# Kernel optimization log

Hardware: AMD Instinct MI355X
Metric: run time of the kernel (lower is better)

The kernel has to match this reference:

```python
import jax, jax.numpy as jnp
import numpy as np

B, N, D_IN = 16, 2048, 256
C, H = 32, 64          # num_capsules, dim_capsules
HEADS, KD = 4, 64      # attention heads, key_dim = dim_capsules
ROUTINGS = 3
EPS_SQ = 1e-7
LN_EPS = 1e-3


def squash(v, axis=-1):
    s2 = jnp.sum(jnp.square(v), axis=axis, keepdims=True)
    scale = s2 / (1.0 + s2) / jnp.sqrt(s2 + EPS_SQ)
    return scale * v


def setup_inputs() -> dict:
    key = jax.random.key(0)
    ks = jax.random.split(key, 10)
    # VarianceScaling(scale=2.0, fan_avg, uniform) for W
    fan_avg = (D_IN + H) / 2.0
    limit = float(np.sqrt(3.0 * 2.0 / fan_avg))
    W = jax.random.uniform(ks[0], (C, D_IN, H), minval=-limit, maxval=limit, dtype=jnp.float32)
    b_caps = jnp.zeros((C, H), jnp.float32)
    gamma = jnp.full((1,), 3.0, jnp.float32)
    x = jax.random.normal(ks[1], (B, N, D_IN), dtype=jnp.float32)
    def glorot(k, shape):
        fin, fout = shape[0], int(np.prod(shape[1:]))
        lim = float(np.sqrt(6.0 / (fin + fout)))
        return jax.random.uniform(k, shape, minval=-lim, maxval=lim, dtype=jnp.float32)
    Wq = glorot(ks[2], (H, HEADS, KD)); bq = jnp.zeros((HEADS, KD), jnp.float32)
    Wk = glorot(ks[3], (H, HEADS, KD)); bk = jnp.zeros((HEADS, KD), jnp.float32)
    Wv = glorot(ks[4], (H, HEADS, KD)); bv = jnp.zeros((HEADS, KD), jnp.float32)
    Wo = glorot(ks[5], (HEADS, KD, H)); bo = jnp.zeros((H,), jnp.float32)
    ln_gamma = jnp.ones((H,), jnp.float32)
    ln_beta = jnp.zeros((H,), jnp.float32)
    return dict(x=x, W=W, b_caps=b_caps, gamma=gamma,
                Wq=Wq, bq=bq, Wk=Wk, bk=bk, Wv=Wv, bv=bv, Wo=Wo, bo=bo,
                ln_gamma=ln_gamma, ln_beta=ln_beta)


def dynamic_routing(u_hat):
    # u_hat: [B, N, C, H]
    b = jnp.zeros(u_hat.shape[:3] + (1,), u_hat.dtype)
    v = None
    for i in range(ROUTINGS):
        c = jax.nn.softmax(b, axis=2)                      # [B,N,C,1]
        s = jnp.sum(c * u_hat, axis=1, keepdims=True)      # [B,1,C,H]
        v = squash(s, axis=-1)
        if i < ROUTINGS - 1:
            agreement = jnp.sum(u_hat * v, axis=-1, keepdims=True)
            b = b + agreement
    return jnp.squeeze(v, axis=1)                          # [B,C,H]


def mha_self(xq, Wq, bq, Wk, bk, Wv, bv, Wo, bo):
    # xq: [B, C, H]
    q = jnp.einsum('bch,hnk->bcnk', xq, Wq) + bq
    k = jnp.einsum('bch,hnk->bcnk', xq, Wk) + bk
    v = jnp.einsum('bch,hnk->bcnk', xq, Wv) + bv
    scores = jnp.einsum('bqnd,bknd->bnqk', q, k) / jnp.sqrt(jnp.asarray(KD, xq.dtype))
    attn = jax.nn.softmax(scores, axis=-1)
    ctx = jnp.einsum('bnqk,bknd->bqnd', attn, v)
    return jnp.einsum('bqnd,ndh->bqh', ctx, Wo) + bo


def reference(x, W, b_caps, gamma, Wq, bq, Wk, bk, Wv, bv, Wo, bo, ln_gamma, ln_beta):
    u_hat = jnp.einsum('bnd,cdh->bnch', x, W) + b_caps[None, None]  # [B,N,C,H]
    routed = dynamic_routing(u_hat)                                  # [B,C,H]
    attended = mha_self(routed, Wq, bq, Wk, bk, Wv, bv, Wo, bo)
    y = attended + routed
    mu = jnp.mean(y, axis=-1, keepdims=True)
    var = jnp.mean(jnp.square(y - mu), axis=-1, keepdims=True)
    routed = (y - mu) / jnp.sqrt(var + LN_EPS) * ln_gamma + ln_beta
    return squash(routed, axis=-1) * gamma
```

## Files before the change

### kernel.cpp

```cpp
#include <hip/hip_runtime.h>
#include <cstddef>

typedef _Float16 f16;
typedef __attribute__((ext_vector_type(4))) _Float16 f16x4;
typedef __attribute__((ext_vector_type(8))) _Float16 f16x8;
typedef __attribute__((ext_vector_type(4))) float f32x4;

namespace {
constexpr int kB = 16;
constexpr int kN = 2048;
constexpr int kD = 256;
constexpr int kC = 32;
constexpr int kH = 64;
constexpr int kHeads = 4;
constexpr int kKD = 64;
constexpr int kChunks = 32;
constexpr int kRows = kN / kChunks;
constexpr int kXJ = 64;

constexpr size_t OFF_XPART = 0;
constexpr size_t OFF_V     = OFF_XPART + 262144;
constexpr size_t OFF_WV    = OFF_V + 32768;
constexpr size_t OFF_BV    = OFF_WV + 131072;
constexpr size_t OFF_Y     = OFF_BV + 512;
constexpr size_t OFF_CS    = OFF_Y + 131072;
constexpr size_t OFF_QKV   = OFF_CS + 512;
constexpr size_t OFF_CTX   = OFF_QKV + 393216;
constexpr size_t OFF_XF16  = OFF_CTX + 524288;
constexpr size_t OFF_WVH   = OFF_XF16 + 4194304;
constexpr size_t OFF_CSP   = OFF_WVH + 65536;
constexpr size_t OFF_YP    = OFF_CSP + 16384;
constexpr size_t WS_NEED_PARTIAL = (OFF_YP + 4194304) * sizeof(float);
}

__global__ __launch_bounds__(256) void k_xpart(const float* __restrict__ x,
                                               float* __restrict__ xpart,
                                               f16* __restrict__ xh) {
  const int b = blockIdx.x, j = blockIdx.y;
  const int t = threadIdx.x;
  const int rg = t >> 6, dq = t & 63;
  __shared__ float sL[4][kD];
  float4 s = {0.f, 0.f, 0.f, 0.f};
  const size_t rowbase = (size_t)b * kN + (size_t)j * 32;
#pragma unroll
  for (int i = 0; i < 8; ++i) {
    const int r = rg * 8 + i;
    const float4 q = *(reinterpret_cast<const float4*>(x + (rowbase + r) * kD) + dq);
    s.x += q.x; s.y += q.y; s.z += q.z; s.w += q.w;
    f16x4 h4 = {(f16)q.x, (f16)q.y, (f16)q.z, (f16)q.w};
    *(reinterpret_cast<f16x4*>(xh + (rowbase + r) * kD) + dq) = h4;
  }
  reinterpret_cast<float4*>(&sL[rg][0])[dq] = s;
  __syncthreads();
  const int d = t;
  xpart[((size_t)b * kXJ + j) * kD + d] =
      sL[0][d] + sL[1][d] + sL[2][d] + sL[3][d];
}

__global__ __launch_bounds__(256) void k_sv(
    const float* __restrict__ W, const float* __restrict__ b_caps,
    const float* __restrict__ xpart, const float* __restrict__ y,
    const float* __restrict__ csum, const float* __restrict__ ypart,
    const float* __restrict__ cspart, float* __restrict__ v,
    float* __restrict__ Wv, f16* __restrict__ Wvh, float* __restrict__ bv,
    const int mode, const int computeWv, const int accWv, const int npart) {
  const int bc = blockIdx.x, b = bc >> 5, c = bc & 31;
  const int t = threadIdx.x;
  const int w = t >> 6, h = t & 63;
  __shared__ float yL[kD];
  __shared__ float sL[4][kH];
  __shared__ float vL[kH];
  __shared__ float csLs;

  if (mode == 0) {
    float s = 0.f;
#pragma unroll 8
    for (int j = 0; j < kXJ; ++j) s += xpart[((size_t)b * kXJ + j) * kD + t];
    yL[t] = s * (1.f / (float)kC);
    if (t == 0) csLs = (float)kN / (float)kC;
  } else if (npart > 0) {
    float s = 0.f;
#pragma unroll 8
    for (int ch = 0; ch < kChunks; ++ch)
      s += ypart[(((size_t)b * kChunks + ch) * kC + c) * kD + t];
    yL[t] = s;
    if (t < 32) {
      float cs_ = cspart[((size_t)b * kChunks + t) * kC + c];
#pragma unroll
      for (int off = 16; off; off >>= 1) cs_ += __shfl_xor(cs_, off, 64);
      if (t == 0) csLs = cs_;
    }
  } else {
    yL[t] = y[(size_t)bc * kD + t];
    if (t == 0) csLs = csum[bc];
  }
  __syncthreads();

  const float* Wc = W + (size_t)c * kD * kH;
  {
    float acc = 0.f;
#pragma unroll 8
    for (int d = w * 64; d < (w + 1) * 64; ++d)
      acc = fmaf(yL[d], Wc[(size_t)d * kH + h], acc);
    sL[w][h] = acc;
  }
  __syncthreads();

  if (t < 64) {
    const float bch = b_caps[c * kH + h];
    float s = sL[0][h] + sL[1][h] + sL[2][h] + sL[3][h] + csLs * bch;
    float s2 = s * s;
#pragma unroll
    for (int off = 32; off; off >>= 1) s2 += __shfl_xor(s2, off, 64);
    const float scale = s2 / (1.f + s2) * rsqrtf(s2 + 1e-7f);
    const float vh = scale * s;
    v[(size_t)bc * kH + h] = vh;
    vL[h] = vh;
    if (computeWv) {
      float bvp = bch * vh;
#pragma unroll
      for (int off = 32; off; off >>= 1) bvp += __shfl_xor(bvp, off, 64);
      if (h == 0) bv[bc] = accWv ? (bv[bc] + bvp) : bvp;
    }
  }
  __syncthreads();
  if (computeWv) {
    float acc = 0.f;
    const float* Wrow = Wc + (size_t)t * kH;
#pragma unroll 8
    for (int hh = 0; hh < kH; ++hh) acc = fmaf(Wrow[hh], vL[hh], acc);
    const size_t idx = (size_t)bc * kD + t;
    const float nv = accWv ? (Wv[idx] + acc) : acc;
    Wv[idx] = nv;
    Wvh[idx] = (f16)nv;
  }
}

__global__ __launch_bounds__(256) void k_route(
    const f16* __restrict__ xh, const f16* __restrict__ Wvh,
    const float* __restrict__ bv, float* __restrict__ y,
    float* __restrict__ csum, float* __restrict__ ypart,
    float* __restrict__ cspart, const int usePart) {
  const int b = blockIdx.x, chunk = blockIdx.y;
  const int t = threadIdx.x;
  const int lane = t & 63, w = t >> 6;
  const int l15 = lane & 15, q = lane >> 4;

  __shared__ __align__(16) f16 xsT[kD][kRows + 8];
  __shared__ float aL[kRows][kC + 4];
  __shared__ __align__(16) f16 pT[kC][kRows + 8];
  __shared__ float csL[8][kC];

  const int n0 = chunk * kRows;
  const float bvc = bv[b * kC + (t & 31)];

  f32x4 acc0 = {0.f, 0.f, 0.f, 0.f}, acc1 = {0.f, 0.f, 0.f, 0.f};
  {
    const int row = w * 16 + l15;
    const f16x8* Ar = reinterpret_cast<const f16x8*>(
        xh + ((size_t)(b * kN + n0 + row)) * kD + q * 8);
    const f16x8* B0 = reinterpret_cast<const f16x8*>(
        Wvh + ((size_t)(b * kC + l15)) * kD + q * 8);
    const f16x8* B1 = reinterpret_cast<const f16x8*>(
        Wvh + ((size_t)(b * kC + 16 + l15)) * kD + q * 8);
#pragma unroll
    for (int ks = 0; ks < 8; ++ks) {
      f16x8 af = Ar[ks * 4];
      acc0 = __builtin_amdgcn_mfma_f32_16x16x32_f16(af, B0[ks * 4], acc0, 0, 0, 0);
      acc1 = __builtin_amdgcn_mfma_f32_16x16x32_f16(af, B1[ks * 4], acc1, 0, 0, 0);
      const int dbase = ks * 32 + q * 8;
#pragma unroll
      for (int i = 0; i < 8; ++i) {
        const int ii = (i + 2 * q) & 7;
        xsT[dbase + ii][row] = af[ii];
      }
    }
  }
#pragma unroll
  for (int r = 0; r < 4; ++r) {
    aL[w * 16 + q * 4 + r][l15] = acc0[r];
    aL[w * 16 + q * 4 + r][16 + l15] = acc1[r];
  }
  __syncthreads();

  const int c = t & 31, sg = t >> 5;
  float csreg = 0.f;
#pragma unroll
  for (int k = 0; k < 8; ++k) {
    const int r = sg * 8 + k;
    float L = bvc + aL[r][c];
    float m = L;
#pragma unroll
    for (int off = 16; off; off >>= 1) m = fmaxf(m, __shfl_xor(m, off, 64));
    const float e = __expf(L - m);
    float ssum = e;
#pragma unroll
    for (int off = 16; off; off >>= 1) ssum += __shfl_xor(ssum, off, 64);
    const float p = e / ssum;
    pT[c][r] = (f16)p;
    csreg += p;
  }
  csL[sg][c] = csreg;
  __syncthreads();

  const int mt2 = w & 1;
  const int ntb = (w >> 1) * 8;
  const f16x8 a0 = *reinterpret_cast<const f16x8*>(&pT[mt2 * 16 + l15][q * 8]);
  const f16x8 a1 = *reinterpret_cast<const f16x8*>(&pT[mt2 * 16 + l15][32 + q * 8]);
  const int cap = mt2 * 16 + q * 4;
#pragma unroll
  for (int i = 0; i < 8; ++i) {
    const int d0 = (ntb + i) * 16;
    const f16x8 b0 = *reinterpret_cast<const f16x8*>(&xsT[d0 + l15][q * 8]);
    const f16x8 b1 = *reinterpret_cast<const f16x8*>(&xsT[d0 + l15][32 + q * 8]);
    f32x4 o = {0.f, 0.f, 0.f, 0.f};
    o = __builtin_amdgcn_mfma_f32_16x16x32_f16(a0, b0, o, 0, 0, 0);
    o = __builtin_amdgcn_mfma_f32_16x16x32_f16(a1, b1, o, 0, 0, 0);
    if (usePart) {
      float* dst = ypart + (((size_t)(b * kChunks + chunk)) * kC + cap) * kD + d0 + l15;
#pragma unroll
      for (int r = 0; r < 4; ++r) dst[(size_t)r * kD] = o[r];
    } else {
      float* dst = y + ((size_t)(b * kC + cap)) * kD + d0 + l15;
#pragma unroll
      for (int r = 0; r < 4; ++r) atomicAdd(dst + (size_t)r * kD, o[r]);
    }
  }
  if (t < 32) {
    float s = 0.f;
#pragma unroll
    for (int j = 0; j < 8; ++j) s += csL[j][t];
    if (usePart) cspart[((size_t)b * kChunks + chunk) * kC + t] = s;
    else atomicAdd(csum + b * kC + t, s);
  }
}

__global__ __launch_bounds__(256) void k_qkv(
    const float* __restrict__ routed, const float* __restrict__ Wq,
    const float* __restrict__ bq, const float* __restrict__ Wk,
    const float* __restrict__ bk, const float* __restrict__ Wvp,
    const float* __restrict__ bvp, float* __restrict__ qkv) {
  const int b = blockIdx.x, head = blockIdx.y, which = blockIdx.z;
  const int t = threadIdx.x;
  const int kk = t & 63, w = t >> 6;
  const float* Wsrc = (which == 0) ? Wq : (which == 1) ? Wk : Wvp;
  const float* bsrc = (which == 0) ? bq : (which == 1) ? bk : bvp;
  __shared__ float rL[kC * kH];
#pragma unroll
  for (int i = 0; i < 8; ++i) rL[t + 256 * i] = routed[(size_t)b * kC * kH + t + 256 * i];
  __syncthreads();
  float acc[8];
  const float bb = bsrc[head * kKD + kk];
#pragma unroll
  for (int i = 0; i < 8; ++i) acc[i] = bb;
#pragma unroll 4
  for (int hh = 0; hh < kH; ++hh) {
    const float wv = Wsrc[((size_t)hh * kHeads + head) * kKD + kk];
#pragma unroll
    for (int i = 0; i < 8; ++i)
      acc[i] = fmaf(rL[(w + 4 * i) * kH + hh], wv, acc[i]);
  }
#pragma unroll
  for (int i = 0; i < 8; ++i) {
    const int cc = w + 4 * i;
    qkv[((((size_t)which * kB + b) * kHeads + head) * kC + cc) * kKD + kk] = acc[i];
  }
}

__global__ __launch_bounds__(256) void k_attn2(const float* __restrict__ qkv,
                                               float* __restrict__ ctx) {
  const int b = blockIdx.x, head = blockIdx.y, t = threadIdx.x;
  constexpr size_t kWhichStride = (size_t)kB * kHeads * kC * kKD;
  const size_t base = ((size_t)b * kHeads + head) * kC * kKD;
  __shared__ float qL[kC][kKD];
  __shared__ float kL[kC][kKD + 1];
  __shared__ float vL[kC][kKD];
  __shared__ float sc[kC][kC + 1];
#pragma unroll
  for (int i = 0; i < 8; ++i) {
    const int e = t + 256 * i, cc = e >> 6, kk = e & 63;
    qL[cc][kk] = qkv[base + e];
    kL[cc][kk] = qkv[base + kWhichStride + e];
    vL[cc][kk] = qkv[base + 2 * kWhichStride + e];
  }
  __syncthreads();
#pragma unroll
  for (int i = 0; i < 4; ++i) {
    const int e = t + 256 * i, qc = e >> 5, kc = e & 31;
    float s = 0.f;
#pragma unroll 8
    for (int d = 0; d < kKD; ++d) s = fmaf(qL[qc][d], kL[kc][d], s);
    sc[qc][kc] = s * 0.125f;
  }
  __syncthreads();
  if (t < kC) {
    float m = -1e30f;
#pragma unroll
    for (int kc = 0; kc < kC; ++kc) m = fmaxf(m, sc[t][kc]);
    float ssum = 0.f;
#pragma unroll
    for (int kc = 0; kc < kC; ++kc) {
      const float e2 = __expf(sc[t][kc] - m);
      sc[t][kc] = e2;
      ssum += e2;
    }
    const float inv = 1.f / ssum;
#pragma unroll
    for (int kc = 0; kc < kC; ++kc) sc[t][kc] *= inv;
  }
  __syncthreads();
#pragma unroll
  for (int i = 0; i < 8; ++i) {
    const int e = t + 256 * i, qc = e >> 6, d = e & 63;
    float s = 0.f;
#pragma unroll 8
    for (int kc = 0; kc < kC; ++kc) s = fmaf(sc[qc][kc], vL[kc][d], s);
    ctx[(((size_t)b * kC + qc) * kHeads + head) * kKD + d] = s;
  }
}

__global__ __launch_bounds__(256) void k_final(
    const float* __restrict__ ctx, const float* __restrict__ Wo,
    const float* __restrict__ bo, const float* __restrict__ routed,
    const float* __restrict__ ln_g, const float* __restrict__ ln_b,
    const float* __restrict__ gamma, float* __restrict__ out) {
  const int bc = blockIdx.x, t = threadIdx.x;
  const int w = t >> 6, h = t & 63;
  __shared__ float cL[kHeads * kKD];
  __shared__ float sL[4][kH];
  cL[t] = ctx[(size_t)bc * (kHeads * kKD) + t];
  __syncthreads();
  float acc = 0.f;
#pragma unroll 8
  for (int nd = w * 64; nd < (w + 1) * 64; ++nd)
    acc = fmaf(cL[nd], Wo[(size_t)nd * kH + h], acc);
  sL[w][h] = acc;
  __syncthreads();
  if (t < 64) {
    const float yv = sL[0][h] + sL[1][h] + sL[2][h] + sL[3][h] + bo[h] +
                     routed[(size_t)bc * kH + h];
    float mu = yv;
#pragma unroll
    for (int off = 32; off; off >>= 1) mu += __shfl_xor(mu, off, 64);
    mu *= (1.f / (float)kH);
    const float dv = yv - mu;
    float var = dv * dv;
#pragma unroll
    for (int off = 32; off; off >>= 1) var += __shfl_xor(var, off, 64);
    var *= (1.f / (float)kH);
    const float nrm = dv * rsqrtf(var + 1e-3f) * ln_g[h] + ln_b[h];
    float s2 = nrm * nrm;
#pragma unroll
    for (int off = 32; off; off >>= 1) s2 += __shfl_xor(s2, off, 64);
    const float scale = s2 / (1.f + s2) * rsqrtf(s2 + 1e-7f);
    out[(size_t)bc * kH + h] = scale * nrm * gamma[0];
  }
}

extern "C" void kernel_launch(void* const* d_in, const int* in_sizes, int n_in,
                              void* d_out, int out_size, void* d_ws, size_t ws_size,
                              hipStream_t stream) {
  (void)in_sizes; (void)n_in; (void)out_size;
  const float* x      = (const float*)d_in[0];
  const float* W      = (const float*)d_in[1];
  const float* b_caps = (const float*)d_in[2];
  const float* gamma  = (const float*)d_in[3];
  const float* Wq     = (const float*)d_in[4];
  const float* bq     = (const float*)d_in[5];
  const float* Wk     = (const float*)d_in[6];
  const float* bk     = (const float*)d_in[7];
  const float* Wv_in  = (const float*)d_in[8];
  const float* bv_in  = (const float*)d_in[9];
  const float* Wo     = (const float*)d_in[10];
  const float* bo     = (const float*)d_in[11];
  const float* ln_g   = (const float*)d_in[12];
  const float* ln_b   = (const float*)d_in[13];
  float* out = (float*)d_out;
  float* ws  = (float*)d_ws;

  float* xpart = ws + OFF_XPART;
  float* v     = ws + OFF_V;
  float* Wv    = ws + OFF_WV;
  float* bv    = ws + OFF_BV;
  float* y     = ws + OFF_Y;
  float* cs    = ws + OFF_CS;
  float* qkv   = ws + OFF_QKV;
  float* ctx   = ws + OFF_CTX;
  f16*   xf16  = (f16*)(ws + OFF_XF16);
  f16*   wvh   = (f16*)(ws + OFF_WVH);
  float* csp   = ws + OFF_CSP;
  float* yp    = ws + OFF_YP;

  const int usePart = (ws_size >= WS_NEED_PARTIAL) ? 1 : 0;

  k_xpart<<<dim3(kB, kXJ), 256, 0, stream>>>(x, xpart, xf16);
  k_sv<<<kB * kC, 256, 0, stream>>>(W, b_caps, xpart, y, cs, yp, csp, v, Wv, wvh, bv,
                                    0, 1, 0, 0);

  if (!usePart) {
    hipMemsetAsync(y, 0, (size_t)kB * kC * kD * sizeof(float), stream);
    hipMemsetAsync(cs, 0, (size_t)kB * kC * sizeof(float), stream);
  }
  k_route<<<dim3(kB, kChunks), 256, 0, stream>>>(xf16, wvh, bv, y, cs, yp, csp, usePart);
  k_sv<<<kB * kC, 256, 0, stream>>>(W, b_caps, xpart, y, cs, yp, csp, v, Wv, wvh, bv,
                                    1, 1, 1,
                                    usePart ? kChunks : 0);

  if (!usePart) {
    hipMemsetAsync(y, 0, (size_t)kB * kC * kD * sizeof(float), stream);
    hipMemsetAsync(cs, 0, (size_t)kB * kC * sizeof(float), stream);
  }
  k_route<<<dim3(kB, kChunks), 256, 0, stream>>>(xf16, wvh, bv, y, cs, yp, csp, usePart);
  k_sv<<<kB * kC, 256, 0, stream>>>(W, b_caps, xpart, y, cs, yp, csp, v, Wv, wvh, bv,
                                    1, 0, 0,
                                    usePart ? kChunks : 0);

  k_qkv<<<dim3(kB, kHeads, 3), 256, 0, stream>>>(v, Wq, bq, Wk, bk, Wv_in, bv_in, qkv);
  k_attn2<<<dim3(kB, kHeads), 256, 0, stream>>>(qkv, ctx);
  k_final<<<kB * kC, 256, 0, stream>>>(ctx, Wo, bo, v, ln_g, ln_b, gamma, out);
}
```

Baseline: 181.7 us.

## Fuse whole capsule pipeline into one cooperative kernel with grid syncs

Replaces the multi-kernel sequence (x partial sums, squash/Wv, two routing passes, QKV, attention, output LN) with a single cooperative kernel of 256 blocks that separates phases with grid.sync. Each block handles two chunks or capsules per phase. The aim is to remove launch overheads and inter-kernel gaps. In exchange, each phase runs on fewer blocks (256 instead of up to 1024), which lowers parallelism and adds grid-barrier cost. The old path stays as a fallback if the cooperative launch fails.

```diff
diff --git a/kernel.cpp b/kernel.cpp
--- a/kernel.cpp
+++ b/kernel.cpp
@@ -1,5 +1,8 @@
 #include <hip/hip_runtime.h>
+#include <hip/hip_cooperative_groups.h>
 #include <cstddef>
+
+namespace cg = cooperative_groups;
 
 typedef _Float16 f16;
 typedef __attribute__((ext_vector_type(4))) _Float16 f16x4;
@@ -31,7 +34,359 @@
 constexpr size_t OFF_CSP   = OFF_WVH + 65536;
 constexpr size_t OFF_YP    = OFF_CSP + 16384;
 constexpr size_t WS_NEED_PARTIAL = (OFF_YP + 4194304) * sizeof(float);
-}
+
+struct SMemRoute {
+  f16 xsT[kD][kRows + 8];
+  float aL[kRows][kC + 4];
+  f16 pT[kC][kRows + 8];
+  float csL[8][kC];
+};
+struct SMemSv {
+  float yL[kD];
+  float sL[4][kH];
+  float vL[kH];
+  float csLs;
+};
+struct SMemAttn {
+  float qL[kC][kKD];
+  float kL[kC][kKD + 1];
+  float vL[kC][kKD];
+  float sc[kC][kC + 1];
+};
+struct SMemMisc {
+  float rL[kC * kH];
+  float red[4][kD];
+  float sL2[4][kH];
+};
+union SMemU {
+  SMemRoute r;
+  SMemSv s;
+  SMemAttn a;
+  SMemMisc m;
+};
+}
+
+
+__device__ __forceinline__ void sv_phase(
+    SMemU& sm, const int b, const int c, const int t,
+    const float* __restrict__ W, const float* __restrict__ b_caps,
+    const float* __restrict__ xpart, const float* __restrict__ ypart,
+    const float* __restrict__ cspart, float* __restrict__ v,
+    float* __restrict__ Wv, f16* __restrict__ Wvh, float* __restrict__ bv,
+    const int mode, const int computeWv, const int accWv) {
+  __syncthreads();
+  const int bc = b * kC + c;
+  const int w = t >> 6, h = t & 63;
+  if (mode == 0) {
+    float s = 0.f;
+#pragma unroll 8
+    for (int j = 0; j < kChunks; ++j) s += xpart[((size_t)b * kChunks + j) * kD + t];
+    sm.s.yL[t] = s * (1.f / (float)kC);
+    if (t == 0) sm.s.csLs = (float)kN / (float)kC;
+  } else {
+    float s = 0.f;
+#pragma unroll 8
+    for (int ch = 0; ch < kChunks; ++ch)
+      s += ypart[(((size_t)b * kChunks + ch) * kC + c) * kD + t];
+    sm.s.yL[t] = s;
+    if (t < 32) {
+      float cs_ = cspart[((size_t)b * kChunks + t) * kC + c];
+#pragma unroll
+      for (int off = 16; off; off >>= 1) cs_ += __shfl_xor(cs_, off, 64);
+      if (t == 0) sm.s.csLs = cs_;
+    }
+  }
+  __syncthreads();
+  const float* Wc = W + (size_t)c * kD * kH;
+  {
+    float acc = 0.f;
+#pragma unroll 8
+    for (int d = w * 64; d < (w + 1) * 64; ++d)
+      acc = fmaf(sm.s.yL[d], Wc[(size_t)d * kH + h], acc);
+    sm.s.sL[w][h] = acc;
+  }
+  __syncthreads();
+  if (t < 64) {
+    const float bch = b_caps[c * kH + h];
+    float s = sm.s.sL[0][h] + sm.s.sL[1][h] + sm.s.sL[2][h] + sm.s.sL[3][h] +
+              sm.s.csLs * bch;
+    float s2 = s * s;
+#pragma unroll
+    for (int off = 32; off; off >>= 1) s2 += __shfl_xor(s2, off, 64);
+    const float scale = s2 / (1.f + s2) * rsqrtf(s2 + 1e-7f);
+    const float vh = scale * s;
+    v[(size_t)bc * kH + h] = vh;
+    sm.s.vL[h] = vh;
+    if (computeWv) {
+      float bvp = bch * vh;
+#pragma unroll
+      for (int off = 32; off; off >>= 1) bvp += __shfl_xor(bvp, off, 64);
+      if (h == 0) bv[bc] = accWv ? (bv[bc] + bvp) : bvp;
+    }
+  }
+  __syncthreads();
+  if (computeWv) {
+    float acc = 0.f;
+    const float* Wrow = Wc + (size_t)t * kH;
+#pragma unroll 8
+    for (int hh = 0; hh < kH; ++hh) acc = fmaf(Wrow[hh], sm.s.vL[hh], acc);
+    const size_t idx = (size_t)bc * kD + t;
+    const float nv = accWv ? (Wv[idx] + acc) : acc;
+    Wv[idx] = nv;
+    Wvh[idx] = (f16)nv;
+  }
+}
+
+__device__ __forceinline__ void route_phase(
+    SMemU& sm, const int b, const int chunk, const int t,
+    const f16* __restrict__ xh, const f16* __restrict__ Wvh,
+    const float* __restrict__ bv, float* __restrict__ ypart,
+    float* __restrict__ cspart) {
+  __syncthreads();
+  const int lane = t & 63, w = t >> 6;
+  const int l15 = lane & 15, q = lane >> 4;
+  const int n0 = chunk * kRows;
+  const float bvc = bv[b * kC + (t & 31)];
+
+  f32x4 acc0 = {0.f, 0.f, 0.f, 0.f}, acc1 = {0.f, 0.f, 0.f, 0.f};
+  {
+    const int row = w * 16 + l15;
+    const f16x8* Ar = reinterpret_cast<const f16x8*>(
+        xh + ((size_t)(b * kN + n0 + row)) * kD + q * 8);
+    const f16x8* B0 = reinterpret_cast<const f16x8*>(
+        Wvh + ((size_t)(b * kC + l15)) * kD + q * 8);
+    const f16x8* B1 = reinterpret_cast<const f16x8*>(
+        Wvh + ((size_t)(b * kC + 16 + l15)) * kD + q * 8);
+#pragma unroll
+    for (int ks = 0; ks < 8; ++ks) {
+      f16x8 af = Ar[ks * 4];
+      acc0 = __builtin_amdgcn_mfma_f32_16x16x32_f16(af, B0[ks * 4], acc0, 0, 0, 0);
+      acc1 = __builtin_amdgcn_mfma_f32_16x16x32_f16(af, B1[ks * 4], acc1, 0, 0, 0);
+      const int dbase = ks * 32 + q * 8;
+#pragma unroll
+      for (int i = 0; i < 8; ++i) {
+        const int ii = (i + 2 * q) & 7;
+        sm.r.xsT[dbase + ii][row] = af[ii];
+      }
+    }
+  }
+#pragma unroll
+  for (int r = 0; r < 4; ++r) {
+    sm.r.aL[w * 16 + q * 4 + r][l15] = acc0[r];
+    sm.r.aL[w * 16 + q * 4 + r][16 + l15] = acc1[r];
+  }
+  __syncthreads();
+
+  const int c = t & 31, sg = t >> 5;
+  float csreg = 0.f;
+#pragma unroll
+  for (int k = 0; k < 8; ++k) {
+    const int r = sg * 8 + k;
+    float L = bvc + sm.r.aL[r][c];
+    float m = L;
+#pragma unroll
+    for (int off = 16; off; off >>= 1) m = fmaxf(m, __shfl_xor(m, off, 64));
+    const float e = __expf(L - m);
+    float ssum = e;
+#pragma unroll
+    for (int off = 16; off; off >>= 1) ssum += __shfl_xor(ssum, off, 64);
+    const float p = e / ssum;
+    sm.r.pT[c][r] = (f16)p;
+    csreg += p;
+  }
+  sm.r.csL[sg][c] = csreg;
+  __syncthreads();
+
+  const int mt2 = w & 1;
+  const int ntb = (w >> 1) * 8;
+  const f16x8 a0 = *reinterpret_cast<const f16x8*>(&sm.r.pT[mt2 * 16 + l15][q * 8]);
+  const f16x8 a1 = *reinterpret_cast<const f16x8*>(&sm.r.pT[mt2 * 16 + l15][32 + q * 8]);
+  const int cap = mt2 * 16 + q * 4;
+#pragma unroll
+  for (int i = 0; i < 8; ++i) {
+    const int d0 = (ntb + i) * 16;
+    const f16x8 b0 = *reinterpret_cast<const f16x8*>(&sm.r.xsT[d0 + l15][q * 8]);
+    const f16x8 b1 = *reinterpret_cast<const f16x8*>(&sm.r.xsT[d0 + l15][32 + q * 8]);
+    f32x4 o = {0.f, 0.f, 0.f, 0.f};
+    o = __builtin_amdgcn_mfma_f32_16x16x32_f16(a0, b0, o, 0, 0, 0);
+    o = __builtin_amdgcn_mfma_f32_16x16x32_f16(a1, b1, o, 0, 0, 0);
+    float* dst = ypart + (((size_t)(b * kChunks + chunk)) * kC + cap) * kD + d0 + l15;
+#pragma unroll
+    for (int r = 0; r < 4; ++r) dst[(size_t)r * kD] = o[r];
+  }
+  if (t < 32) {
+    float s = 0.f;
+#pragma unroll
+    for (int j = 0; j < 8; ++j) s += sm.r.csL[j][t];
+    cspart[((size_t)b * kChunks + chunk) * kC + t] = s;
+  }
+}
+
+__global__ __launch_bounds__(256) void k_caps(
+    const float* __restrict__ x, const float* __restrict__ W,
+    const float* __restrict__ b_caps, const float* __restrict__ Wq,
+    const float* __restrict__ bq, const float* __restrict__ Wk,
+    const float* __restrict__ bk, const float* __restrict__ Wvp,
+    const float* __restrict__ bvp, const float* __restrict__ Wo,
+    const float* __restrict__ bo, const float* __restrict__ ln_g,
+    const float* __restrict__ ln_b, const float* __restrict__ gamma,
+    float* __restrict__ xpart, float* __restrict__ v, float* __restrict__ Wv,
+    f16* __restrict__ Wvh, float* __restrict__ bv, f16* __restrict__ xh,
+    float* __restrict__ ypart, float* __restrict__ cspart,
+    float* __restrict__ qkv, float* __restrict__ ctx, float* __restrict__ out) {
+  cg::grid_group grid = cg::this_grid();
+  __shared__ __align__(16) SMemU sm;
+  const int blk = blockIdx.x;
+  const int b = blk >> 4, g16 = blk & 15;
+  const int t = threadIdx.x;
+
+  for (int u = 0; u < 2; ++u) {
+    __syncthreads();
+    const int chunk = g16 * 2 + u;
+    const int rg = t >> 6, dq = t & 63;
+    float4 s = {0.f, 0.f, 0.f, 0.f};
+    const size_t rowbase = (size_t)b * kN + (size_t)chunk * kRows;
+#pragma unroll
+    for (int i = 0; i < 16; ++i) {
+      const int r = rg * 16 + i;
+      const float4 qv = *(reinterpret_cast<const float4*>(x + (rowbase + r) * kD) + dq);
+      s.x += qv.x; s.y += qv.y; s.z += qv.z; s.w += qv.w;
+      f16x4 h4 = {(f16)qv.x, (f16)qv.y, (f16)qv.z, (f16)qv.w};
+      *(reinterpret_cast<f16x4*>(xh + (rowbase + r) * kD) + dq) = h4;
+    }
+    reinterpret_cast<float4*>(&sm.m.red[rg][0])[dq] = s;
+    __syncthreads();
+    xpart[((size_t)b * kChunks + chunk) * kD + t] =
+        sm.m.red[0][t] + sm.m.red[1][t] + sm.m.red[2][t] + sm.m.red[3][t];
+  }
+  grid.sync();
+  for (int u = 0; u < 2; ++u)
+    sv_phase(sm, b, g16 * 2 + u, t, W, b_caps, xpart, ypart, cspart, v, Wv, Wvh,
+             bv, 0, 1, 0);
+  grid.sync();
+  for (int u = 0; u < 2; ++u)
+    route_phase(sm, b, g16 * 2 + u, t, xh, Wvh, bv, ypart, cspart);
+  grid.sync();
+  for (int u = 0; u < 2; ++u)
+    sv_phase(sm, b, g16 * 2 + u, t, W, b_caps, xpart, ypart, cspart, v, Wv, Wvh,
+             bv, 1, 1, 1);
+  grid.sync();
+  for (int u = 0; u < 2; ++u)
+    route_phase(sm, b, g16 * 2 + u, t, xh, Wvh, bv, ypart, cspart);
+  grid.sync();
+  for (int u = 0; u < 2; ++u)
+    sv_phase(sm, b, g16 * 2 + u, t, W, b_caps, xpart, ypart, cspart, v, Wv, Wvh,
+             bv, 1, 0, 0);
+  grid.sync();
+  if (blk < 192) {
+    const int which = blk >> 6, rem = blk & 63;
+    const int b2 = rem >> 2, head = rem & 3;
+    const int kk = t & 63, w2 = t >> 6;
+    const float* Wsrc = (which == 0) ? Wq : (which == 1) ? Wk : Wvp;
+    const float* bsrc = (which == 0) ? bq : (which == 1) ? bk : bvp;
+#pragma unroll
+    for (int i = 0; i < 8; ++i)
+      sm.m.rL[t + 256 * i] = v[(size_t)b2 * kC * kH + t + 256 * i];
+    __syncthreads();
+    float acc[8];
+    const float bb = bsrc[head * kKD + kk];
+#pragma unroll
+    for (int i = 0; i < 8; ++i) acc[i] = bb;
+#pragma unroll 4
+    for (int hh = 0; hh < kH; ++hh) {
+      const float wv = Wsrc[((size_t)hh * kHeads + head) * kKD + kk];
+#pragma unroll
+      for (int i = 0; i < 8; ++i)
+        acc[i] = fmaf(sm.m.rL[(w2 + 4 * i) * kH + hh], wv, acc[i]);
+    }
+#pragma unroll
+    for (int i = 0; i < 8; ++i) {
+      const int cc = w2 + 4 * i;
+      qkv[((((size_t)which * kB + b2) * kHeads + head) * kC + cc) * kKD + kk] = acc[i];
+    }
+  }
+  grid.sync();
+  if (blk < 64) {
+    const int b2 = blk >> 2, head = blk & 3;
+    constexpr size_t kWhichStride = (size_t)kB * kHeads * kC * kKD;
+    const size_t base = ((size_t)b2 * kHeads + head) * kC * kKD;
+#pragma unroll
+    for (int i = 0; i < 8; ++i) {
+      const int e = t + 256 * i, cc = e >> 6, kk = e & 63;
+      sm.a.qL[cc][kk] = qkv[base + e];
+      sm.a.kL[cc][kk] = qkv[base + kWhichStride + e];
+      sm.a.vL[cc][kk] = qkv[base + 2 * kWhichStride + e];
+    }
+    __syncthreads();
+#pragma unroll
+    for (int i = 0; i < 4; ++i) {
+      const int e = t + 256 * i, qc = e >> 5, kc = e & 31;
+      float s = 0.f;
+#pragma unroll 8
+      for (int d = 0; d < kKD; ++d) s = fmaf(sm.a.qL[qc][d], sm.a.kL[kc][d], s);
+      sm.a.sc[qc][kc] = s * 0.125f;
+    }
+    __syncthreads();
+    if (t < kC) {
+      float m = -1e30f;
+#pragma unroll
+      for (int kc = 0; kc < kC; ++kc) m = fmaxf(m, sm.a.sc[t][kc]);
+      float ssum = 0.f;
+#pragma unroll
+      for (int kc = 0; kc < kC; ++kc) {
+        const float e2 = __expf(sm.a.sc[t][kc] - m);
+        sm.a.sc[t][kc] = e2;
+        ssum += e2;
+      }
+      const float inv = 1.f / ssum;
+#pragma unroll
+      for (int kc = 0; kc < kC; ++kc) sm.a.sc[t][kc] *= inv;
+    }
+    __syncthreads();
+#pragma unroll
+    for (int i = 0; i < 8; ++i) {
+      const int e = t + 256 * i, qc = e >> 6, d = e & 63;
+      float s = 0.f;
+#pragma unroll 8
+      for (int kc = 0; kc < kC; ++kc) s = fmaf(sm.a.sc[qc][kc], sm.a.vL[kc][d], s);
+      ctx[(((size_t)b2 * kC + qc) * kHeads + head) * kKD + d] = s;
+    }
+  }
+  grid.sync();
+  for (int u = 0; u < 2; ++u) {
+    __syncthreads();
+    const int bc = blk * 2 + u;
+    const int w2 = t >> 6, h = t & 63;
+    sm.m.rL[t] = ctx[(size_t)bc * (kHeads * kKD) + t];
+    __syncthreads();
+    float acc = 0.f;
+#pragma unroll 8
+    for (int nd = w2 * 64; nd < (w2 + 1) * 64; ++nd)
+      acc = fmaf(sm.m.rL[nd], Wo[(size_t)nd * kH + h], acc);
+    sm.m.sL2[w2][h] = acc;
+    __syncthreads();
+    if (t < 64) {
+      const float yv = sm.m.sL2[0][h] + sm.m.sL2[1][h] + sm.m.sL2[2][h] +
+                       sm.m.sL2[3][h] + bo[h] + v[(size_t)bc * kH + h];
+      float mu = yv;
+#pragma unroll
+      for (int off = 32; off; off >>= 1) mu += __shfl_xor(mu, off, 64);
+      mu *= (1.f / (float)kH);
+      const float dv = yv - mu;
+      float var = dv * dv;
+#pragma unroll
+      for (int off = 32; off; off >>= 1) var += __shfl_xor(var, off, 64);
+      var *= (1.f / (float)kH);
+      const float nrm = dv * rsqrtf(var + 1e-3f) * ln_g[h] + ln_b[h];
+      float s2 = nrm * nrm;
+#pragma unroll
+      for (int off = 32; off; off >>= 1) s2 += __shfl_xor(s2, off, 64);
+      const float scale = s2 / (1.f + s2) * rsqrtf(s2 + 1e-7f);
+      out[(size_t)bc * kH + h] = scale * nrm * gamma[0];
+    }
+  }
+}
+
 
 __global__ __launch_bounds__(256) void k_xpart(const float* __restrict__ x,
                                                float* __restrict__ xpart,
@@ -393,6 +748,25 @@
 
   const int usePart = (ws_size >= WS_NEED_PARTIAL) ? 1 : 0;
 
+  hipError_t cerr = hipErrorUnknown;
+  if (usePart) {
+    int dev = 0, coopAttr = 0;
+    hipGetDevice(&dev);
+    hipDeviceGetAttribute(&coopAttr, hipDeviceAttributeCooperativeLaunch, dev);
+    if (coopAttr) {
+      void* args[] = {
+          (void*)&x, (void*)&W, (void*)&b_caps, (void*)&Wq, (void*)&bq,
+          (void*)&Wk, (void*)&bk, (void*)&Wv_in, (void*)&bv_in, (void*)&Wo,
+          (void*)&bo, (void*)&ln_g, (void*)&ln_b, (void*)&gamma,
+          (void*)&xpart, (void*)&v, (void*)&Wv, (void*)&wvh, (void*)&bv,
+          (void*)&xf16, (void*)&yp, (void*)&csp, (void*)&qkv, (void*)&ctx,
+          (void*)&out};
+      cerr = hipLaunchCooperativeKernel((const void*)k_caps, dim3(256), dim3(256),
+                                        args, 0, stream);
+    }
+  }
+  if (cerr == hipSuccess) return;
+
   k_xpart<<<dim3(kB, kXJ), 256, 0, stream>>>(x, xpart, xf16);
   k_sv<<<kB * kC, 256, 0, stream>>>(W, b_caps, xpart, y, cs, yp, csp, v, Wv, wvh, bv,
                                     0, 1, 0, 0);
```

New measurement: 448.8 us. +147.0%, slower.
